# Kernel tuning notes

Hardware: AMD Instinct MI355X
Metric: run time of the kernel (lower is better)

The kernel has to match this reference:

```python
import jax, jax.numpy as jnp
import numpy as np

I, H = 64, 128
C = 2 * I + H  # concat(x, h, mask) feature dim
_SIZES = [H * C, H, H * C, H, H * C, H, I * I, I, H * I, H, H, 1]
_OFFS = np.cumsum([0] + _SIZES)


def _unpack(params):
    nf = params.shape[0]
    seg = lambda i, shape: params[:, _OFFS[i]:_OFFS[i + 1]].reshape((nf,) + shape)
    zw, zb = seg(0, (H, C)), seg(1, (H,))
    rw, rb = seg(2, (H, C)), seg(3, (H,))
    hw, hb = seg(4, (H, C)), seg(5, (H,))
    gxw, gxb = seg(6, (I, I)), seg(7, (I,))
    ghw, ghb = seg(8, (H, I)), seg(9, (H,))
    fcw, fcb = seg(10, (H,)), seg(11, (1,))
    # FilterLinear mask is identity -> only the diagonal of gamma_x_l.weight matters
    gxd = jnp.diagonal(gxw, axis1=1, axis2=2)  # [nf, I]
    return zw, zb, rw, rb, hw, hb, gxd, gxb, ghw, ghb, fcw, fcb


def setup_inputs() -> dict:
    key = jax.random.key(0)
    ks = jax.random.split(key, 6)
    nf, B, T = 64, 128, 100
    params = jax.random.normal(ks[0], (nf, int(_OFFS[-1])), jnp.float32) * 0.05
    X = jax.random.normal(ks[1], (B, T, I), jnp.float32)
    X_last_obsv = jax.random.normal(ks[2], (B, T, I), jnp.float32)
    x_mean = jax.random.normal(ks[3], (1, T, I), jnp.float32)
    Mask = jax.random.bernoulli(ks[4], 0.5, (nf, B, T, I)).astype(jnp.float32)
    Delta = jax.random.uniform(ks[5], (nf, B, T, I), jnp.float32) * 5.0
    return {"params": params, "X": X, "X_last_obsv": X_last_obsv,
            "x_mean": x_mean, "Mask": Mask, "Delta": Delta}


def reference(params, X, X_last_obsv, x_mean, Mask, Delta):
    zw, zb, rw, rb, hw, hb, gxd, gxb, ghw, ghb, fcw, fcb = _unpack(params)
    nf = params.shape[0]
    B = X.shape[0]
    h0 = jnp.zeros((nf, B, H), X.dtype)
    # scan over time: xs leading axis = T
    xs = (X.transpose(1, 0, 2),            # [T, B, I]
          X_last_obsv.transpose(1, 0, 2),  # [T, B, I]
          x_mean[0],                       # [T, I]
          Mask.transpose(2, 0, 1, 3),      # [T, nf, B, I]
          Delta.transpose(2, 0, 1, 3))     # [T, nf, B, I]

    def step(h, inp):
        x_t, xl_t, xm_t, m_t, d_t = inp
        # gamma_x (diagonal FilterLinear): exp(-relu(W_diag * delta + b))
        delta_x = jnp.exp(-jax.nn.relu(d_t * gxd[:, None, :] + gxb[:, None, :]))
        delta_h = jnp.exp(-jax.nn.relu(
            jnp.einsum('nbi,nhi->nbh', d_t, ghw) + ghb[:, None, :]))
        x = m_t * x_t[None] + (1.0 - m_t) * (
            delta_x * xl_t[None] + (1.0 - delta_x) * xm_t[None, None, :])
        h = delta_h * h
        comb = jnp.concatenate([x, h, m_t], axis=-1)            # [nf, B, C]
        z = jax.nn.sigmoid(jnp.einsum('nbc,nhc->nbh', comb, zw) + zb[:, None])
        r = jax.nn.sigmoid(jnp.einsum('nbc,nhc->nbh', comb, rw) + rb[:, None])
        comb2 = jnp.concatenate([x, r * h, m_t], axis=-1)
        h_tilde = jnp.tanh(jnp.einsum('nbc,nhc->nbh', comb2, hw) + hb[:, None])
        h = (1.0 - z) * h + z * h_tilde
        return h, None

    h, _ = jax.lax.scan(step, h0, xs)
    # fc + sigmoid (dropout in eval mode = identity)
    out = jax.nn.sigmoid(jnp.einsum('nbh,nh->nb', h, fcw) + fcb)  # fcb [nf,1] broadcasts
    return out[..., None]  # [nf, B, 1]
```

## Files before the change

kernel.cpp:

```cpp
#include <hip/hip_runtime.h>

#define NF 64
#define BATCH 128
#define TT 100
#define II 64
#define HH 128
#define CC 256
#define BB 32
#define NTHR 512
#define PSTRIDE 111297

#define OFF_ZW 0
#define OFF_ZB 32768
#define OFF_RW 32896
#define OFF_RB 65664
#define OFF_HW 65792
#define OFF_HB 98560
#define OFF_GXW 98688
#define OFF_GXB 102784
#define OFF_GHW 102848
#define OFF_GHB 111040
#define OFF_FCW 111168
#define OFF_FCB 111296

#define ZR_PER_N 65536
#define H_BASE   (64 * ZR_PER_N)
#define H_PER_N  32768
#define G_BASE   (H_BASE + 64 * H_PER_N)
#define G_PER_N  8192
#define WS_ELEMS (G_BASE + 64 * G_PER_N)

typedef __bf16 bf16x8 __attribute__((ext_vector_type(8)));
typedef __bf16 bf16x4 __attribute__((ext_vector_type(4)));
typedef float f32x4 __attribute__((ext_vector_type(4)));

__device__ __forceinline__ f32x4 mfma16(bf16x8 a, bf16x8 b, f32x4 c) {
  return __builtin_amdgcn_mfma_f32_16x16x32_bf16(a, b, c, 0, 0, 0);
}
__device__ __forceinline__ float rcpf_(float x) { return __builtin_amdgcn_rcpf(x); }
__device__ __forceinline__ float sigmoidf_(float x) { return rcpf_(1.f + __expf(-x)); }
__device__ __forceinline__ float tanhf_(float x) {
  float e = __expf(-2.f * __builtin_fabsf(x));
  float t = (1.f - e) * rcpf_(1.f + e);
  return x < 0.f ? -t : t;
}
__device__ __forceinline__ int SW(int x) { return x ^ (((x >> 4) & 3) << 1); }

#define XA(par, mt, kt)  ((((par)*2 + (mt)) * 2 + (kt)) * 512)
#define MAPL(par, mt, kt) (4096 + XA(par, mt, kt))
#define DAH(mt, kt) (8192 + (((mt)*2 + (kt)) * 512))
#define HAH(mt, q) (10240 + (((mt)*4 + (q)) * 512))
#define RHH(mt, q) (14336 + (((mt)*4 + (q)) * 512))
#define POOL_ELEMS 18432

__global__ void repack_kernel(const float* __restrict__ p, __bf16* __restrict__ ws) {
  const int total = 4194304 + 2097152 + 524288;
  for (int e = blockIdx.x * 256 + threadIdx.x; e < total; e += gridDim.x * 256) {
    float wv; int dst;
    if (e < 4194304) {
      int j = e & 7, l = (e >> 3) & 63, nt = (e >> 9) & 15, kt = (e >> 13) & 7, n = e >> 16;
      int c = kt * 32 + (l >> 4) * 8 + j, l15 = l & 15;
      long pn = (long)n * PSTRIDE;
      wv = (nt < 8) ? p[pn + OFF_ZW + (nt * 16 + l15) * CC + c]
                    : p[pn + OFF_RW + ((nt - 8) * 16 + l15) * CC + c];
      dst = n * ZR_PER_N + (kt * 16 + nt) * 512 + l * 8 + j;
    } else if (e < 4194304 + 2097152) {
      int e2 = e - 4194304;
      int j = e2 & 7, l = (e2 >> 3) & 63, nt = (e2 >> 9) & 7, kt = (e2 >> 12) & 7, n = e2 >> 15;
      int c = kt * 32 + (l >> 4) * 8 + j, l15 = l & 15;
      wv = p[(long)n * PSTRIDE + OFF_HW + (nt * 16 + l15) * CC + c];
      dst = H_BASE + n * H_PER_N + (kt * 8 + nt) * 512 + l * 8 + j;
    } else {
      int e2 = e - (4194304 + 2097152);
      int j = e2 & 7, l = (e2 >> 3) & 63, nt = (e2 >> 9) & 7, kt = (e2 >> 12) & 1, n = e2 >> 13;
      int c = kt * 32 + (l >> 4) * 8 + j, l15 = l & 15;
      wv = p[(long)n * PSTRIDE + OFF_GHW + (nt * 16 + l15) * II + c];
      dst = G_BASE + n * G_PER_N + (kt * 8 + nt) * 512 + l * 8 + j;
    }
    ws[dst] = (__bf16)wv;
  }
}

__global__ __launch_bounds__(NTHR, 2) void grud_main(
    const float* __restrict__ p, const float* __restrict__ X,
    const float* __restrict__ XL, const float* __restrict__ XM,
    const float* __restrict__ MK, const float* __restrict__ DE,
    const __bf16* __restrict__ ws, float* __restrict__ out) {
  __shared__ __align__(16) __bf16 pool[POOL_ELEMS];

  const int tid = threadIdx.x;
  const int w = tid >> 6, l = tid & 63;
  const int l15 = l & 15, lg = l >> 4;
  const int n = blockIdx.x & 63;
  const int b0 = (blockIdx.x >> 6) * BB;
  const long pn = (long)n * PSTRIDE;
  const int cw = w * 16 + l15;
  const int sl = SW(l);

  bf16x8 wgR[2], wzR[8], wrR[8], whR[8];
  {
    const __bf16* wzr = ws + n * ZR_PER_N;
    const __bf16* wh_ = ws + H_BASE + n * H_PER_N;
    const __bf16* wg_ = ws + G_BASE + n * G_PER_N;
#pragma unroll
    for (int kt = 0; kt < 2; ++kt)
      wgR[kt] = *(const bf16x8*)(wg_ + (kt * 8 + w) * 512 + l * 8);
#pragma unroll
    for (int kt = 0; kt < 8; ++kt) {
      wzR[kt] = *(const bf16x8*)(wzr + (kt * 16 + w) * 512 + l * 8);
      wrR[kt] = *(const bf16x8*)(wzr + (kt * 16 + 8 + w) * 512 + l * 8);
      whR[kt] = *(const bf16x8*)(wh_ + (kt * 8 + w) * 512 + l * 8);
    }
  }

  const float zb = p[pn + OFF_ZB + cw];
  const float rb = p[pn + OFF_RB + cw];
  const float hb = p[pn + OFF_HB + cw];
  const float gb = p[pn + OFF_GHB + cw];
  const f32x4 zb4 = {zb, zb, zb, zb};
  const f32x4 rb4 = {rb, rb, rb, rb};
  const f32x4 hb4 = {hb, hb, hb, hb};
  const f32x4 gb4 = {gb, gb, gb, gb};

  const int hq = ((64 + cw) >> 5) - 2;
  const int qh = (cw >> 3) & 3;
  const int hj = cw & 7;
  int hsrow[4];
#pragma unroll
  for (int r = 0; r < 4; ++r) hsrow[r] = qh * 16 + ((lg * 4 + r) ^ (qh << 1));

  const int arow = tid >> 4;
  const int ai0 = (tid & 15) * 4;
  const int amt = arow >> 4;
  const int akt = ai0 >> 5;
  const int salane = SW(((ai0 >> 3) & 3) * 16 + (arow & 15));
  const int aj = ai0 & 7;
  const float* __restrict__ Xp  = X  + (long)(b0 + arow) * TT * II + ai0;
  const float* __restrict__ XLp = XL + (long)(b0 + arow) * TT * II + ai0;
  const float* __restrict__ MKp = MK + ((long)(n * BATCH + b0 + arow) * TT) * II + ai0;
  const float* __restrict__ DEp = DE + ((long)(n * BATCH + b0 + arow) * TT) * II + ai0;
  float gxd4[4], gxb4v[4];
#pragma unroll
  for (int u = 0; u < 4; ++u) {
    gxd4[u] = p[pn + OFF_GXW + (ai0 + u) * 65];
    gxb4v[u] = p[pn + OFF_GXB + ai0 + u];
  }

  float h[2][4] = {{0.f, 0.f, 0.f, 0.f}, {0.f, 0.f, 0.f, 0.f}};

  for (int e = tid; e < 4096; e += NTHR) pool[10240 + e] = (__bf16)0.f;

  f32x4 fx  = *(const f32x4*)Xp;
  f32x4 fxl = *(const f32x4*)XLp;
  f32x4 fxm = *(const f32x4*)(XM + ai0);
  f32x4 fm  = __builtin_nontemporal_load((const f32x4*)MKp);
  f32x4 fd  = __builtin_nontemporal_load((const f32x4*)DEp);
  {
    bf16x4 xh, mh;
#pragma unroll
    for (int u = 0; u < 4; ++u) {
      float m = fm[u], d = fd[u];
      float dx = __expf(-fmaxf(fmaf(d, gxd4[u], gxb4v[u]), 0.f));
      float b = fmaf(dx, fxl[u] - fxm[u], fxm[u]);
      float xv = fmaf(m, fx[u] - b, b);
      xh[u] = (__bf16)xv;
      mh[u] = (__bf16)m;
    }
    *(bf16x4*)&pool[XA(0, amt, akt) + salane * 8 + aj] = xh;
    *(bf16x4*)&pool[MAPL(0, amt, akt) + salane * 8 + aj] = mh;
  }
  {
    const long to = (long)(TT > 1 ? 1 : 0) * II;
    fx  = *(const f32x4*)(Xp + to);
    fxl = *(const f32x4*)(XLp + to);
    fxm = *(const f32x4*)(XM + to + ai0);
    fm  = __builtin_nontemporal_load((const f32x4*)(MKp + to));
    fd  = __builtin_nontemporal_load((const f32x4*)(DEp + to));
  }
  __syncthreads();

  for (int t = 0; t < TT; ++t) {
    const int par = t & 1, parn = par ^ 1;
    const bool more = (t + 1 < TT);

    if (more) {
      bf16x4 xh, mh, dh;
#pragma unroll
      for (int u = 0; u < 4; ++u) {
        float m = fm[u], d = fd[u];
        float dx = __expf(-fmaxf(fmaf(d, gxd4[u], gxb4v[u]), 0.f));
        float b = fmaf(dx, fxl[u] - fxm[u], fxm[u]);
        float xv = fmaf(m, fx[u] - b, b);
        xh[u] = (__bf16)xv;
        mh[u] = (__bf16)m;
        dh[u] = (__bf16)d;
      }
      *(bf16x4*)&pool[XA(parn, amt, akt) + salane * 8 + aj] = xh;
      *(bf16x4*)&pool[MAPL(parn, amt, akt) + salane * 8 + aj] = mh;
      *(bf16x4*)&pool[DAH(amt, akt) + salane * 8 + aj] = dh;
      const long to = (long)(t + 2 < TT ? t + 2 : TT - 1) * II;
      fx  = *(const f32x4*)(Xp + to);
      fxl = *(const f32x4*)(XLp + to);
      fxm = *(const f32x4*)(XM + to + ai0);
      fm  = __builtin_nontemporal_load((const f32x4*)(MKp + to));
      fd  = __builtin_nontemporal_load((const f32x4*)(DEp + to));
    }

    float zv[2][4];
#pragma unroll
    for (int mt = 0; mt < 2; ++mt) {
      f32x4 az = zb4, ar = rb4;
#pragma unroll
      for (int kt = 0; kt < 8; ++kt) {
        const __bf16* ahp = (kt < 2) ? &pool[XA(par, mt, kt) + sl * 8]
                          : (kt < 6) ? &pool[HAH(mt, kt - 2) + sl * 8]
                                     : &pool[MAPL(par, mt, kt - 6) + sl * 8];
        bf16x8 ah = *(const bf16x8*)ahp;
        az = mfma16(ah, wzR[kt], az);
        ar = mfma16(ah, wrR[kt], ar);
      }
#pragma unroll
      for (int r = 0; r < 4; ++r) {
        zv[mt][r] = sigmoidf_(az[r]);
        float rv = sigmoidf_(ar[r]);
        float rh = rv * h[mt][r];
        pool[RHH(mt, hq) + hsrow[r] * 8 + hj] = (__bf16)rh;
      }
    }
    __syncthreads();

#pragma unroll
    for (int mt = 0; mt < 2; ++mt) {
      f32x4 ahh = hb4;
#pragma unroll
      for (int kt = 0; kt < 8; ++kt) {
        const __bf16* ahp = (kt < 2) ? &pool[XA(par, mt, kt) + sl * 8]
                          : (kt < 6) ? &pool[RHH(mt, kt - 2) + sl * 8]
                                     : &pool[MAPL(par, mt, kt - 6) + sl * 8];
        bf16x8 ah = *(const bf16x8*)ahp;
        ahh = mfma16(ah, whR[kt], ahh);
      }
      f32x4 ad = gb4;
      if (more) {
#pragma unroll
        for (int kt = 0; kt < 2; ++kt) {
          bf16x8 ah = *(const bf16x8*)&pool[DAH(mt, kt) + sl * 8];
          ad = mfma16(ah, wgR[kt], ad);
        }
      }
#pragma unroll
      for (int r = 0; r < 4; ++r) {
        float ht = tanhf_(ahh[r]);
        float hn = fmaf(zv[mt][r], ht - h[mt][r], h[mt][r]);
        if (more) {
          hn *= __expf(-fmaxf(ad[r], 0.f));
          pool[HAH(mt, hq) + hsrow[r] * 8 + hj] = (__bf16)hn;
        }
        h[mt][r] = hn;
      }
    }
    __syncthreads();
  }

  float* hst = (float*)pool;
#pragma unroll
  for (int mt = 0; mt < 2; ++mt)
#pragma unroll
    for (int r = 0; r < 4; ++r) hst[(mt * 16 + lg * 4 + r) * 132 + cw] = h[mt][r];
  __syncthreads();
  if (tid < BB) {
    float acc = p[pn + OFF_FCB];
    for (int j = 0; j < HH; ++j) acc = fmaf(hst[tid * 132 + j], p[pn + OFF_FCW + j], acc);
    out[n * BATCH + b0 + tid] = sigmoidf_(acc);
  }
}

extern "C" void kernel_launch(void* const* d_in, const int* in_sizes, int n_in,
                              void* d_out, int out_size, void* d_ws, size_t ws_size,
                              hipStream_t stream) {
  const float* p  = (const float*)d_in[0];
  const float* X  = (const float*)d_in[1];
  const float* XL = (const float*)d_in[2];
  const float* XM = (const float*)d_in[3];
  const float* MK = (const float*)d_in[4];
  const float* DE = (const float*)d_in[5];
  float* out = (float*)d_out;
  __bf16* ws = (__bf16*)d_ws;
  if (ws_size < (size_t)WS_ELEMS * 2) return;

  hipLaunchKernelGGL(repack_kernel, dim3(4096), dim3(256), 0, stream, p, ws);
  hipLaunchKernelGGL(grud_main, dim3(NF * (BATCH / BB)), dim3(NTHR), 0, stream,
                     p, X, XL, XM, MK, DE, ws, out);
}
```

Before: 247.3 us.

## Precompute x/mask gate contributions off the recurrent critical path

Splits the z/r/h̃ MFMA accumulations into the h-independent part (x and mask columns) and the recurrent part. The x/mask part for step t+1 is computed during phase two of step t, and the h̃ x/mask part during phase one, so the work between barriers that depends on h shrinks. Tanh is also simplified to a single exp/rcp form. This costs extra accumulator registers per thread and may reduce occupancy, and the new tanh can overflow for large negative inputs (rcp of inf gives 0, which still yields -1).

```diff
diff --git a/kernel.cpp b/kernel.cpp
--- a/kernel.cpp
+++ b/kernel.cpp
@@ -40,9 +40,7 @@
 __device__ __forceinline__ float rcpf_(float x) { return __builtin_amdgcn_rcpf(x); }
 __device__ __forceinline__ float sigmoidf_(float x) { return rcpf_(1.f + __expf(-x)); }
 __device__ __forceinline__ float tanhf_(float x) {
-  float e = __expf(-2.f * __builtin_fabsf(x));
-  float t = (1.f - e) * rcpf_(1.f + e);
-  return x < 0.f ? -t : t;
+  return fmaf(2.f, rcpf_(1.f + __expf(-2.f * x)), -1.f);
 }
 __device__ __forceinline__ int SW(int x) { return x ^ (((x >> 4) & 3) << 1); }
 
@@ -147,6 +145,8 @@
   }
 
   float h[2][4] = {{0.f, 0.f, 0.f, 0.f}, {0.f, 0.f, 0.f, 0.f}};
+  f32x4 azp[2], arp[2];
+  f32x4 ahp[2];
 
   for (int e = tid; e < 4096; e += NTHR) pool[10240 + e] = (__bf16)0.f;
 
@@ -178,6 +178,24 @@
     fd  = __builtin_nontemporal_load((const f32x4*)(DEp + to));
   }
   __syncthreads();
+
+#pragma unroll
+  for (int mt = 0; mt < 2; ++mt) {
+    f32x4 az = zb4, ar = rb4;
+#pragma unroll
+    for (int kt = 0; kt < 2; ++kt) {
+      bf16x8 ah = *(const bf16x8*)&pool[XA(0, mt, kt) + sl * 8];
+      az = mfma16(ah, wzR[kt], az);
+      ar = mfma16(ah, wrR[kt], ar);
+    }
+#pragma unroll
+    for (int kt = 6; kt < 8; ++kt) {
+      bf16x8 ah = *(const bf16x8*)&pool[MAPL(0, mt, kt - 6) + sl * 8];
+      az = mfma16(ah, wzR[kt], az);
+      ar = mfma16(ah, wrR[kt], ar);
+    }
+    azp[mt] = az; arp[mt] = ar;
+  }
 
   for (int t = 0; t < TT; ++t) {
     const int par = t & 1, parn = par ^ 1;
@@ -209,16 +227,25 @@
     float zv[2][4];
 #pragma unroll
     for (int mt = 0; mt < 2; ++mt) {
-      f32x4 az = zb4, ar = rb4;
-#pragma unroll
-      for (int kt = 0; kt < 8; ++kt) {
-        const __bf16* ahp = (kt < 2) ? &pool[XA(par, mt, kt) + sl * 8]
-                          : (kt < 6) ? &pool[HAH(mt, kt - 2) + sl * 8]
-                                     : &pool[MAPL(par, mt, kt - 6) + sl * 8];
-        bf16x8 ah = *(const bf16x8*)ahp;
+      f32x4 az = azp[mt], ar = arp[mt];
+#pragma unroll
+      for (int kt = 2; kt < 6; ++kt) {
+        bf16x8 ah = *(const bf16x8*)&pool[HAH(mt, kt - 2) + sl * 8];
         az = mfma16(ah, wzR[kt], az);
         ar = mfma16(ah, wrR[kt], ar);
       }
+      f32x4 ahh = hb4;
+#pragma unroll
+      for (int kt = 0; kt < 2; ++kt) {
+        bf16x8 ah = *(const bf16x8*)&pool[XA(par, mt, kt) + sl * 8];
+        ahh = mfma16(ah, whR[kt], ahh);
+      }
+#pragma unroll
+      for (int kt = 6; kt < 8; ++kt) {
+        bf16x8 ah = *(const bf16x8*)&pool[MAPL(par, mt, kt - 6) + sl * 8];
+        ahh = mfma16(ah, whR[kt], ahh);
+      }
+      ahp[mt] = ahh;
 #pragma unroll
       for (int r = 0; r < 4; ++r) {
         zv[mt][r] = sigmoidf_(az[r]);
@@ -231,13 +258,10 @@
 
 #pragma unroll
     for (int mt = 0; mt < 2; ++mt) {
-      f32x4 ahh = hb4;
-#pragma unroll
-      for (int kt = 0; kt < 8; ++kt) {
-        const __bf16* ahp = (kt < 2) ? &pool[XA(par, mt, kt) + sl * 8]
-                          : (kt < 6) ? &pool[RHH(mt, kt - 2) + sl * 8]
-                                     : &pool[MAPL(par, mt, kt - 6) + sl * 8];
-        bf16x8 ah = *(const bf16x8*)ahp;
+      f32x4 ahh = ahp[mt];
+#pragma unroll
+      for (int kt = 2; kt < 6; ++kt) {
+        bf16x8 ah = *(const bf16x8*)&pool[RHH(mt, kt - 2) + sl * 8];
         ahh = mfma16(ah, whR[kt], ahh);
       }
       f32x4 ad = gb4;
@@ -247,6 +271,20 @@
           bf16x8 ah = *(const bf16x8*)&pool[DAH(mt, kt) + sl * 8];
           ad = mfma16(ah, wgR[kt], ad);
         }
+        f32x4 az = zb4, ar = rb4;
+#pragma unroll
+        for (int kt = 0; kt < 2; ++kt) {
+          bf16x8 ah = *(const bf16x8*)&pool[XA(parn, mt, kt) + sl * 8];
+          az = mfma16(ah, wzR[kt], az);
+          ar = mfma16(ah, wrR[kt], ar);
+        }
+#pragma unroll
+        for (int kt = 6; kt < 8; ++kt) {
+          bf16x8 ah = *(const bf16x8*)&pool[MAPL(parn, mt, kt - 6) + sl * 8];
+          az = mfma16(ah, wzR[kt], az);
+          ar = mfma16(ah, wrR[kt], ar);
+        }
+        azp[mt] = az; arp[mt] = ar;
       }
 #pragma unroll
       for (int r = 0; r < 4; ++r) {
```

Measured after the change: 242.8 us. About the same (-1.8%).
